# Performance work log

Hardware: AMD Instinct MI355X
Metric: run time of the kernel (lower is better)

Reference implementation:

```python
import jax, jax.numpy as jnp
import numpy as np

BS, SL, H, DH = 2, 2048, 32, 128
STRIDE = 16
NUM_PAGES = BS * (SL // STRIDE)  # 256, distinct page per block
PAGE_DIM = 1 * 2 * STRIDE * H * DH  # blocks * partitions * stride * kv_heads * head_dim


def setup_inputs() -> dict:
    key = jax.random.key(0)
    k1, k2, k3 = jax.random.split(key, 3)
    xq = jax.random.normal(k1, (BS, SL, H, DH), dtype=jnp.float32)
    xk = jax.random.normal(k2, (BS, SL, H, DH), dtype=jnp.float32)
    xv = jax.random.normal(k3, (BS, SL, H, DH), dtype=jnp.float32)
    cache_state = jnp.zeros((NUM_PAGES, PAGE_DIM), dtype=jnp.float32)
    seq_block_ids = jnp.arange(BS * (SL // STRIDE), dtype=jnp.int64 if jax.config.jax_enable_x64 else jnp.int32).reshape(BS, SL // STRIDE)
    return {"xq": xq, "xk": xk, "xv": xv, "cache_state": cache_state, "seq_block_ids": seq_block_ids}


def reference(xq, xk, xv, cache_state, seq_block_ids):
    bs, sl, h, dh = xq.shape
    nb = sl // STRIDE  # blocks per sequence
    num_pages = cache_state.shape[0]

    # --- paged cache write (prefill path: start_positions is None) ---
    # page layout: [page, transformer_block(=1), partition(k=0,v=1), stride, head, head_dim]
    cache = cache_state.reshape(num_pages, 1, 2, STRIDE, h, dh)
    pids = seq_block_ids.reshape(-1)  # [bs*nb]
    k_blocks = xk.reshape(bs * nb, STRIDE, h, dh)
    v_blocks = xv.reshape(bs * nb, STRIDE, h, dh)
    cache = cache.at[pids, 0, 0].set(k_blocks)
    cache = cache.at[pids, 0, 1].set(v_blocks)
    new_cache_state = cache.reshape(cache_state.shape)

    # --- GQA repeat_kv: n_rep = head_count // head_count_kv = 1 -> no-op ---

    # --- SDPA, attn_mask=None, is_causal=False ---
    scale = 1.0 / np.sqrt(dh).astype(np.float32)
    scores = jnp.einsum("bqhd,bkhd->bhqk", xq, xk) * scale  # [bs, h, sl, sl]
    attn = jax.nn.softmax(scores, axis=-1)
    out = jnp.einsum("bhqk,bkhd->bqhd", attn, xv)
    attn_output = out.reshape(bs, sl, h * dh)
    return attn_output, new_cache_state
```

## Files before the change

kernel.cpp:

```cpp
#include <hip/hip_runtime.h>
#include <hip/hip_bf16.h>
#include <stdint.h>

#define BS 2
#define SL 2048
#define H 32
#define DH 128
#define ATT_ELEMS (BS*SL*H*DH)
#define KTILES (SL/64)
#define QSCALE (0.08838834764831845f * 1.4426950408889634f)

typedef __attribute__((ext_vector_type(8))) short short8_t;
typedef __attribute__((ext_vector_type(16))) float f32x16_t;
typedef __attribute__((ext_vector_type(4))) unsigned int u32x4_t;
typedef __attribute__((ext_vector_type(2))) unsigned int u32x2_t;

union FragU { u32x4_t u; short8_t s; };

__device__ __forceinline__ unsigned short f2bf(float x){
    union { float f; unsigned int u; } v; v.f = x;
    unsigned int r = v.u + 0x7fffu + ((v.u >> 16) & 1u);
    return (unsigned short)(r >> 16);
}
__device__ __forceinline__ unsigned int pack2(float a, float b){
    return (unsigned int)f2bf(a) | ((unsigned int)f2bf(b) << 16);
}
__device__ __forceinline__ unsigned int cvtpk(float a, float b){
    unsigned int r;
    asm("v_cvt_pk_bf16_f32 %0, %1, %2" : "=v"(r) : "v"(a), "v"(b));
    return r;
}
__device__ __forceinline__ void gload16(const unsigned short* g, unsigned short* l){
    __builtin_amdgcn_global_load_lds(
        (const __attribute__((address_space(1))) void*)(const void*)g,
        (__attribute__((address_space(3))) void*)(void*)l, 16, 0, 0);
}

__global__ __launch_bounds__(256) void prep_kv_kernel(const float* __restrict__ xk,
                                                      const float* __restrict__ xv,
                                                      const int* __restrict__ pids,
                                                      unsigned short* __restrict__ kfr,
                                                      unsigned short* __restrict__ vfr,
                                                      float* __restrict__ out_cache,
                                                      int do_cache){
    __shared__ unsigned short tK[64*136];
    __shared__ unsigned short tV[64*136];
    int tile = blockIdx.x, h = blockIdx.y, b = blockIdx.z;
    int tid = threadIdx.x;
    size_t tbase = ((size_t)((b*H + h)*KTILES + tile)) * 8192;
    int pg[4];
    #pragma unroll
    for (int j = 0; j < 4; ++j) pg[j] = pids[b*128 + tile*4 + j];

    #pragma unroll
    for (int i = 0; i < 8; ++i){
        int c = tid + 256*i;
        int row = c >> 5, f4 = c & 31;
        size_t gidx = ((size_t)((b*SL + tile*64 + row)*H + h))*DH + f4*4;
        float4 kx = *(const float4*)(xk + gidx);
        float4 vx = *(const float4*)(xv + gidx);
        u32x2_t kw; kw[0] = pack2(kx.x, kx.y); kw[1] = pack2(kx.z, kx.w);
        u32x2_t vw; vw[0] = pack2(vx.x, vx.y); vw[1] = pack2(vx.z, vx.w);
        *(u32x2_t*)(&tK[row*136 + f4*4]) = kw;
        *(u32x2_t*)(&tV[row*136 + f4*4]) = vw;
        if (do_cache){
            size_t cb = (size_t)pg[row>>4]*131072 + (size_t)(row&15)*4096 + h*128 + f4*4;
            *(float4*)(out_cache + cb)         = kx;
            *(float4*)(out_cache + cb + 65536) = vx;
        }
    }
    __syncthreads();
    #pragma unroll
    for (int i = 0; i < 4; ++i){
        int c = tid + 256*i;
        int fi = c >> 6, l = c & 63;
        int key = (fi >> 3)*32 + (l & 31);
        int d0  = (fi & 7)*16 + (l >> 5)*8;
        u32x4_t w = *(const u32x4_t*)(&tK[key*136 + d0]);
        *(u32x4_t*)(&kfr[tbase + (size_t)c*8]) = w;
    }
    #pragma unroll
    for (int i = 0; i < 4; ++i){
        int c = tid + 256*i;
        int fi = c >> 6, l = c & 63;
        int d  = (fi >> 2)*32 + (l & 31);
        int k0 = (fi & 3)*16 + (l >> 5)*8;
        u32x4_t u;
        #pragma unroll
        for (int w = 0; w < 4; ++w)
            u[w] = (unsigned)tV[(k0+2*w)*136 + d] | ((unsigned)tV[(k0+2*w+1)*136 + d] << 16);
        *(u32x4_t*)(&vfr[tbase + (size_t)c*8]) = u;
    }
}

__global__ __launch_bounds__(256) void cache_scatter_kernel(const float* __restrict__ xk,
                                                            const float* __restrict__ xv,
                                                            const int* __restrict__ pids,
                                                            float* __restrict__ out_cache){
    int sb = blockIdx.x >> 1, part = blockIdx.x & 1;
    int page = pids[sb];
    const float4* s4 = (const float4*)((part ? xv : xk) + (size_t)sb * 65536);
    float4* d4 = (float4*)(out_cache + (size_t)page * 131072 + (size_t)part * 65536);
    int base = blockIdx.y * 2048 + threadIdx.x;
    #pragma unroll
    for (int i = 0; i < 8; ++i) d4[base + i*256] = s4[base + i*256];
}

__global__ __launch_bounds__(256, 2) void attn_kernel(const float* __restrict__ xq,
                                                      const unsigned short* __restrict__ kfr,
                                                      const unsigned short* __restrict__ vfr,
                                                      float* __restrict__ out){
    __shared__ unsigned short smem[4*8192];

    const int tid  = threadIdx.x;
    const int lane = tid & 63;
    const int wave = tid >> 6;
    const int l31  = lane & 31;
    const int hi   = lane >> 5;

    int lin = blockIdx.x;
    int swz = (lin & 7)*128 + (lin >> 3);
    const int qblk = swz & 15;
    const int h    = (swz >> 4) & 31;
    const int b    = swz >> 9;
    const int qbase = qblk*128 + wave*32;

    short8_t qf[8];
    {
        const float* qptr = xq + ((size_t)((b*SL + qbase + l31)*H + h))*DH + hi*8;
        #pragma unroll
        for (int f = 0; f < 8; ++f){
            float4 a = *(const float4*)(qptr + f*16);
            float4 c = *(const float4*)(qptr + f*16 + 4);
            FragU w;
            w.u[0] = pack2(a.x*QSCALE, a.y*QSCALE);
            w.u[1] = pack2(a.z*QSCALE, a.w*QSCALE);
            w.u[2] = pack2(c.x*QSCALE, c.y*QSCALE);
            w.u[3] = pack2(c.z*QSCALE, c.w*QSCALE);
            qf[f] = w.s;
        }
    }

    f32x16_t acc[4];
    #pragma unroll
    for (int d = 0; d < 4; ++d)
        #pragma unroll
        for (int r = 0; r < 16; ++r) acc[d][r] = 0.f;
    float m = -1e30f, l_run = 0.f;

    const size_t bh = (size_t)(b*H + h) * (KTILES*8192);
    const unsigned short* kg = kfr + bh;
    const unsigned short* vg = vfr + bh;

    #pragma unroll
    for (int i = 0; i < 4; ++i){
        int ch = wave*4 + i;
        gload16(kg + ch*512 + lane*8, smem + ch*512);
        gload16(vg + ch*512 + lane*8, smem + 16384 + ch*512);
    }
    asm volatile("s_waitcnt vmcnt(0)" ::: "memory");
    __builtin_amdgcn_s_barrier();
    asm volatile("" ::: "memory");

    #pragma unroll 1
    for (int t = 0; t < KTILES; ++t){
        const int p = t & 1;
        unsigned short* Kc = smem + p*8192;
        unsigned short* Vc = smem + 16384 + p*8192;

        if (t + 1 < KTILES){
            const unsigned short* kn = kg + (size_t)(t+1)*8192;
            const unsigned short* vn = vg + (size_t)(t+1)*8192;
            unsigned short* Kn = smem + (p^1)*8192;
            unsigned short* Vn = smem + 16384 + (p^1)*8192;
            #pragma unroll
            for (int i = 0; i < 4; ++i){
                int ch = wave*4 + i;
                gload16(kn + ch*512 + lane*8, Kn + ch*512);
                gload16(vn + ch*512 + lane*8, Vn + ch*512);
            }
        }
        __builtin_amdgcn_sched_barrier(0);

        f32x16_t s0a, s0b, s1a, s1b;
        #pragma unroll
        for (int r = 0; r < 16; ++r){ s0a[r] = 0.f; s0b[r] = 0.f; s1a[r] = 0.f; s1b[r] = 0.f; }
        __builtin_amdgcn_s_setprio(1);
        #pragma unroll
        for (int f = 0; f < 4; ++f){
            FragU k0, k1, k2, k3;
            k0.u = *(const u32x4_t*)(&Kc[(f   )*512 + lane*8]);
            k1.u = *(const u32x4_t*)(&Kc[(8+f )*512 + lane*8]);
            k2.u = *(const u32x4_t*)(&Kc[(4+f )*512 + lane*8]);
            k3.u = *(const u32x4_t*)(&Kc[(12+f)*512 + lane*8]);
            s0a = __builtin_amdgcn_mfma_f32_32x32x16_bf16(k0.s, qf[f],   s0a, 0, 0, 0);
            s1a = __builtin_amdgcn_mfma_f32_32x32x16_bf16(k1.s, qf[f],   s1a, 0, 0, 0);
            s0b = __builtin_amdgcn_mfma_f32_32x32x16_bf16(k2.s, qf[4+f], s0b, 0, 0, 0);
            s1b = __builtin_amdgcn_mfma_f32_32x32x16_bf16(k3.s, qf[4+f], s1b, 0, 0, 0);
        }
        __builtin_amdgcn_s_setprio(0);
        f32x16_t s0 = s0a + s0b;
        f32x16_t s1 = s1a + s1b;

        float t16[16];
        #pragma unroll
        for (int r = 0; r < 16; ++r) t16[r] = fmaxf(s0[r], s1[r]);
        #pragma unroll
        for (int w = 8; w >= 1; w >>= 1)
            #pragma unroll
            for (int r = 0; r < 8; ++r)
                if (r < w) t16[r] = fmaxf(t16[r], t16[r+w]);
        float tmax = fmaxf(t16[0], __shfl_xor(t16[0], 32, 64));

        if (!__all(tmax - m <= 8.f)){
            float mn = fmaxf(m, tmax);
            float corr = __builtin_amdgcn_exp2f(m - mn);
            l_run *= corr;
            float cr[16];
            #pragma unroll
            for (int r = 0; r < 16; ++r)
                cr[r] = __shfl(corr, (r&3) + 8*(r>>2) + 4*hi, 64);
            #pragma unroll
            for (int d = 0; d < 4; ++d)
                #pragma unroll
                for (int r = 0; r < 16; ++r) acc[d][r] *= cr[r];
            m = mn;
        }

        float lsum = 0.f;
        FragU pf[4];
        #define PSLICE(KS, SV, RB)                                                          \
        {                                                                                   \
            float e0 = __builtin_amdgcn_exp2f(SV[RB+0] - m);                                \
            float e1 = __builtin_amdgcn_exp2f(SV[RB+1] - m);                                \
            float e2 = __builtin_amdgcn_exp2f(SV[RB+2] - m);                                \
            float e3 = __builtin_amdgcn_exp2f(SV[RB+3] - m);                                \
            float e4 = __builtin_amdgcn_exp2f(SV[RB+4] - m);                                \
            float e5 = __builtin_amdgcn_exp2f(SV[RB+5] - m);                                \
            float e6 = __builtin_amdgcn_exp2f(SV[RB+6] - m);                                \
            float e7 = __builtin_amdgcn_exp2f(SV[RB+7] - m);                                \
            lsum += ((e0+e1)+(e2+e3)) + ((e4+e5)+(e6+e7));                                  \
            unsigned a  = cvtpk(e0,e1), bq = cvtpk(e2,e3);                                  \
            unsigned cq = cvtpk(e4,e5), dq = cvtpk(e6,e7);                                  \
            unsigned y0 = hi ? a : cq,  y1 = hi ? bq : dq;                                  \
            unsigned r0 = __shfl_xor(y0, 32, 64);                                           \
            unsigned r1 = __shfl_xor(y1, 32, 64);                                           \
            pf[KS].u[0] = hi ? r0 : a;  pf[KS].u[1] = hi ? r1 : bq;                         \
            pf[KS].u[2] = hi ? cq : r0; pf[KS].u[3] = hi ? dq : r1;                         \
        }
        PSLICE(0, s0, 0)
        PSLICE(1, s0, 8)
        PSLICE(2, s1, 0)
        PSLICE(3, s1, 8)
        #undef PSLICE
        lsum += __shfl_xor(lsum, 32, 64);
        l_run += lsum;

        __builtin_amdgcn_s_setprio(1);
        #pragma unroll
        for (int dblk = 0; dblk < 4; ++dblk){
            #pragma unroll
            for (int ks = 0; ks < 4; ++ks){
                FragU vb;
                vb.u = *(const u32x4_t*)(&Vc[(dblk*4 + ks)*512 + lane*8]);
                acc[dblk] = __builtin_amdgcn_mfma_f32_32x32x16_bf16(pf[ks].s, vb.s, acc[dblk], 0, 0, 0);
            }
        }
        __builtin_amdgcn_s_setprio(0);

        if (t + 1 < KTILES){
            asm volatile("s_waitcnt vmcnt(0)" ::: "memory");
            __builtin_amdgcn_s_barrier();
            asm volatile("" ::: "memory");
        }
    }

    float linv = 1.f / l_run;
    float lr[16];
    #pragma unroll
    for (int r = 0; r < 16; ++r)
        lr[r] = __shfl(linv, (r&3) + 8*(r>>2) + 4*hi, 64);
    #pragma unroll
    for (int dblk = 0; dblk < 4; ++dblk){
        #pragma unroll
        for (int r = 0; r < 16; ++r){
            int q = qbase + (r&3) + 8*(r>>2) + 4*hi;
            out[(size_t)(b*SL + q)*(H*DH) + h*DH + dblk*32 + l31] = acc[dblk][r] * lr[r];
        }
    }
}

extern "C" void kernel_launch(void* const* d_in, const int* in_sizes, int n_in,
                              void* d_out, int out_size, void* d_ws, size_t ws_size,
                              hipStream_t stream) {
    const float* xq = (const float*)d_in[0];
    const float* xk = (const float*)d_in[1];
    const float* xv = (const float*)d_in[2];
    const int* pids = (const int*)d_in[4];

    float* out_attn  = (float*)d_out;
    float* out_cache = out_attn + (size_t)ATT_ELEMS;

    const size_t frag_elems = (size_t)BS*H*KTILES*8192;
    const size_t need       = 2*frag_elems*sizeof(unsigned short);

    if (ws_size >= need){
        unsigned short* kfr = (unsigned short*)d_ws;
        unsigned short* vfr = kfr + frag_elems;
        prep_kv_kernel<<<dim3(KTILES, H, BS), 256, 0, stream>>>(xk, xv, pids, kfr, vfr, out_cache, 1);
        attn_kernel<<<dim3(BS*H*(SL/128)), 256, 0, stream>>>(xq, kfr, vfr, out_attn);
    } else {
        unsigned short* vfr = (unsigned short*)out_cache;
        unsigned short* kfr = vfr + frag_elems;
        prep_kv_kernel<<<dim3(KTILES, H, BS), 256, 0, stream>>>(xk, xv, pids, kfr, vfr, out_cache, 0);
        attn_kernel<<<dim3(BS*H*(SL/128)), 256, 0, stream>>>(xq, kfr, vfr, out_attn);
        cache_scatter_kernel<<<dim3(512, 8), 256, 0, stream>>>(xk, xv, pids, out_cache);
    }
}
```

Measured before the change: 236.5 us.

## Halve attention key tile to 32 and raise occupancy to four blocks per CU

Attention now processes keys in tiles of 32 instead of 64, halving the shared-memory double buffer and the score and probability register arrays. Launch bounds move from 2 to 4 blocks per CU, aiming to hide latency through occupancy. The prep kernel's fragment layout is rearranged so each 64-key tile holds two contiguous 32-key sub-tiles. In exchange there are twice as many loop iterations, so more barriers, more softmax max-reductions and more rescale checks per key, and registers may spill under the tighter bound.

```diff
diff --git a/kernel.cpp b/kernel.cpp
--- a/kernel.cpp
+++ b/kernel.cpp
@@ -8,6 +8,7 @@
 #define DH 128
 #define ATT_ELEMS (BS*SL*H*DH)
 #define KTILES (SL/64)
+#define KT32 (SL/32)
 #define QSCALE (0.08838834764831845f * 1.4426950408889634f)
 
 typedef __attribute__((ext_vector_type(8))) short short8_t;
@@ -47,7 +48,7 @@
     __shared__ unsigned short tV[64*136];
     int tile = blockIdx.x, h = blockIdx.y, b = blockIdx.z;
     int tid = threadIdx.x;
-    size_t tbase = ((size_t)((b*H + h)*KTILES + tile)) * 8192;
+    size_t tb = ((size_t)((b*H + h)*KTILES + tile)) * 8192;
     int pg[4];
     #pragma unroll
     for (int j = 0; j < 4; ++j) pg[j] = pids[b*128 + tile*4 + j];
@@ -73,23 +74,25 @@
     #pragma unroll
     for (int i = 0; i < 4; ++i){
         int c = tid + 256*i;
-        int fi = c >> 6, l = c & 63;
-        int key = (fi >> 3)*32 + (l & 31);
-        int d0  = (fi & 7)*16 + (l >> 5)*8;
+        int sub = c >> 9, c2 = c & 511;
+        int fi = c2 >> 6, l = c2 & 63;
+        int key = sub*32 + (l & 31);
+        int d0  = fi*16 + (l >> 5)*8;
         u32x4_t w = *(const u32x4_t*)(&tK[key*136 + d0]);
-        *(u32x4_t*)(&kfr[tbase + (size_t)c*8]) = w;
+        *(u32x4_t*)(&kfr[tb + (size_t)sub*4096 + (size_t)c2*8]) = w;
     }
     #pragma unroll
     for (int i = 0; i < 4; ++i){
         int c = tid + 256*i;
-        int fi = c >> 6, l = c & 63;
-        int d  = (fi >> 2)*32 + (l & 31);
-        int k0 = (fi & 3)*16 + (l >> 5)*8;
+        int sub = c >> 9, c2 = c & 511;
+        int fi = c2 >> 6, l = c2 & 63;
+        int d  = (fi >> 1)*32 + (l & 31);
+        int k0 = sub*32 + (fi & 1)*16 + (l >> 5)*8;
         u32x4_t u;
         #pragma unroll
         for (int w = 0; w < 4; ++w)
             u[w] = (unsigned)tV[(k0+2*w)*136 + d] | ((unsigned)tV[(k0+2*w+1)*136 + d] << 16);
-        *(u32x4_t*)(&vfr[tbase + (size_t)c*8]) = u;
+        *(u32x4_t*)(&vfr[tb + (size_t)sub*4096 + (size_t)c2*8]) = u;
     }
 }
 
@@ -106,11 +109,11 @@
     for (int i = 0; i < 8; ++i) d4[base + i*256] = s4[base + i*256];
 }
 
-__global__ __launch_bounds__(256, 2) void attn_kernel(const float* __restrict__ xq,
+__global__ __launch_bounds__(256, 4) void attn_kernel(const float* __restrict__ xq,
                                                       const unsigned short* __restrict__ kfr,
                                                       const unsigned short* __restrict__ vfr,
                                                       float* __restrict__ out){
-    __shared__ unsigned short smem[4*8192];
+    __shared__ unsigned short smem[4*4096];
 
     const int tid  = threadIdx.x;
     const int lane = tid & 63;
@@ -148,69 +151,64 @@
         for (int r = 0; r < 16; ++r) acc[d][r] = 0.f;
     float m = -1e30f, l_run = 0.f;
 
-    const size_t bh = (size_t)(b*H + h) * (KTILES*8192);
+    const size_t bh = (size_t)(b*H + h) * ((size_t)KT32*4096);
     const unsigned short* kg = kfr + bh;
     const unsigned short* vg = vfr + bh;
 
     #pragma unroll
-    for (int i = 0; i < 4; ++i){
-        int ch = wave*4 + i;
+    for (int i = 0; i < 2; ++i){
+        int ch = wave*2 + i;
         gload16(kg + ch*512 + lane*8, smem + ch*512);
-        gload16(vg + ch*512 + lane*8, smem + 16384 + ch*512);
+        gload16(vg + ch*512 + lane*8, smem + 8192 + ch*512);
     }
     asm volatile("s_waitcnt vmcnt(0)" ::: "memory");
     __builtin_amdgcn_s_barrier();
     asm volatile("" ::: "memory");
 
     #pragma unroll 1
-    for (int t = 0; t < KTILES; ++t){
+    for (int t = 0; t < KT32; ++t){
         const int p = t & 1;
-        unsigned short* Kc = smem + p*8192;
-        unsigned short* Vc = smem + 16384 + p*8192;
-
-        if (t + 1 < KTILES){
-            const unsigned short* kn = kg + (size_t)(t+1)*8192;
-            const unsigned short* vn = vg + (size_t)(t+1)*8192;
-            unsigned short* Kn = smem + (p^1)*8192;
-            unsigned short* Vn = smem + 16384 + (p^1)*8192;
-            #pragma unroll
-            for (int i = 0; i < 4; ++i){
-                int ch = wave*4 + i;
+        unsigned short* Kc = smem + p*4096;
+        unsigned short* Vc = smem + 8192 + p*4096;
+
+        if (t + 1 < KT32){
+            const unsigned short* kn = kg + (size_t)(t+1)*4096;
+            const unsigned short* vn = vg + (size_t)(t+1)*4096;
+            unsigned short* Kn = smem + (p^1)*4096;
+            unsigned short* Vn = smem + 8192 + (p^1)*4096;
+            #pragma unroll
+            for (int i = 0; i < 2; ++i){
+                int ch = wave*2 + i;
                 gload16(kn + ch*512 + lane*8, Kn + ch*512);
                 gload16(vn + ch*512 + lane*8, Vn + ch*512);
             }
         }
         __builtin_amdgcn_sched_barrier(0);
 
-        f32x16_t s0a, s0b, s1a, s1b;
-        #pragma unroll
-        for (int r = 0; r < 16; ++r){ s0a[r] = 0.f; s0b[r] = 0.f; s1a[r] = 0.f; s1b[r] = 0.f; }
+        f32x16_t sa, sb;
+        #pragma unroll
+        for (int r = 0; r < 16; ++r){ sa[r] = 0.f; sb[r] = 0.f; }
         __builtin_amdgcn_s_setprio(1);
         #pragma unroll
         for (int f = 0; f < 4; ++f){
-            FragU k0, k1, k2, k3;
-            k0.u = *(const u32x4_t*)(&Kc[(f   )*512 + lane*8]);
-            k1.u = *(const u32x4_t*)(&Kc[(8+f )*512 + lane*8]);
-            k2.u = *(const u32x4_t*)(&Kc[(4+f )*512 + lane*8]);
-            k3.u = *(const u32x4_t*)(&Kc[(12+f)*512 + lane*8]);
-            s0a = __builtin_amdgcn_mfma_f32_32x32x16_bf16(k0.s, qf[f],   s0a, 0, 0, 0);
-            s1a = __builtin_amdgcn_mfma_f32_32x32x16_bf16(k1.s, qf[f],   s1a, 0, 0, 0);
-            s0b = __builtin_amdgcn_mfma_f32_32x32x16_bf16(k2.s, qf[4+f], s0b, 0, 0, 0);
-            s1b = __builtin_amdgcn_mfma_f32_32x32x16_bf16(k3.s, qf[4+f], s1b, 0, 0, 0);
+            FragU k0, k1;
+            k0.u = *(const u32x4_t*)(&Kc[(f  )*512 + lane*8]);
+            k1.u = *(const u32x4_t*)(&Kc[(4+f)*512 + lane*8]);
+            sa = __builtin_amdgcn_mfma_f32_32x32x16_bf16(k0.s, qf[f],   sa, 0, 0, 0);
+            sb = __builtin_amdgcn_mfma_f32_32x32x16_bf16(k1.s, qf[4+f], sb, 0, 0, 0);
         }
         __builtin_amdgcn_s_setprio(0);
-        f32x16_t s0 = s0a + s0b;
-        f32x16_t s1 = s1a + s1b;
-
-        float t16[16];
-        #pragma unroll
-        for (int r = 0; r < 16; ++r) t16[r] = fmaxf(s0[r], s1[r]);
-        #pragma unroll
-        for (int w = 8; w >= 1; w >>= 1)
-            #pragma unroll
-            for (int r = 0; r < 8; ++r)
-                if (r < w) t16[r] = fmaxf(t16[r], t16[r+w]);
-        float tmax = fmaxf(t16[0], __shfl_xor(t16[0], 32, 64));
+        f32x16_t s = sa + sb;
+
+        float t8[8];
+        #pragma unroll
+        for (int r = 0; r < 8; ++r) t8[r] = fmaxf(s[r], s[8+r]);
+        #pragma unroll
+        for (int w = 4; w >= 1; w >>= 1)
+            #pragma unroll
+            for (int r = 0; r < 4; ++r)
+                if (r < w) t8[r] = fmaxf(t8[r], t8[r+w]);
+        float tmax = fmaxf(t8[0], __shfl_xor(t8[0], 32, 64));
 
         if (!__all(tmax - m <= 8.f)){
             float mn = fmaxf(m, tmax);
@@ -228,17 +226,17 @@
         }
 
         float lsum = 0.f;
-        FragU pf[4];
-        #define PSLICE(KS, SV, RB)                                                          \
+        FragU pf[2];
+        #define PSLICE(KS, RB)                                                              \
         {                                                                                   \
-            float e0 = __builtin_amdgcn_exp2f(SV[RB+0] - m);                                \
-            float e1 = __builtin_amdgcn_exp2f(SV[RB+1] - m);                                \
-            float e2 = __builtin_amdgcn_exp2f(SV[RB+2] - m);                                \
-            float e3 = __builtin_amdgcn_exp2f(SV[RB+3] - m);                                \
-            float e4 = __builtin_amdgcn_exp2f(SV[RB+4] - m);                                \
-            float e5 = __builtin_amdgcn_exp2f(SV[RB+5] - m);                                \
-            float e6 = __builtin_amdgcn_exp2f(SV[RB+6] - m);                                \
-            float e7 = __builtin_amdgcn_exp2f(SV[RB+7] - m);                                \
+            float e0 = __builtin_amdgcn_exp2f(s[RB+0] - m);                                 \
+            float e1 = __builtin_amdgcn_exp2f(s[RB+1] - m);                                 \
+            float e2 = __builtin_amdgcn_exp2f(s[RB+2] - m);                                 \
+            float e3 = __builtin_amdgcn_exp2f(s[RB+3] - m);                                 \
+            float e4 = __builtin_amdgcn_exp2f(s[RB+4] - m);                                 \
+            float e5 = __builtin_amdgcn_exp2f(s[RB+5] - m);                                 \
+            float e6 = __builtin_amdgcn_exp2f(s[RB+6] - m);                                 \
+            float e7 = __builtin_amdgcn_exp2f(s[RB+7] - m);                                 \
             lsum += ((e0+e1)+(e2+e3)) + ((e4+e5)+(e6+e7));                                  \
             unsigned a  = cvtpk(e0,e1), bq = cvtpk(e2,e3);                                  \
             unsigned cq = cvtpk(e4,e5), dq = cvtpk(e6,e7);                                  \
@@ -248,10 +246,8 @@
             pf[KS].u[0] = hi ? r0 : a;  pf[KS].u[1] = hi ? r1 : bq;                         \
             pf[KS].u[2] = hi ? cq : r0; pf[KS].u[3] = hi ? dq : r1;                         \
         }
-        PSLICE(0, s0, 0)
-        PSLICE(1, s0, 8)
-        PSLICE(2, s1, 0)
-        PSLICE(3, s1, 8)
+        PSLICE(0, 0)
+        PSLICE(1, 8)
         #undef PSLICE
         lsum += __shfl_xor(lsum, 32, 64);
         l_run += lsum;
@@ -260,15 +256,15 @@
         #pragma unroll
         for (int dblk = 0; dblk < 4; ++dblk){
             #pragma unroll
-            for (int ks = 0; ks < 4; ++ks){
+            for (int ks = 0; ks < 2; ++ks){
                 FragU vb;
-                vb.u = *(const u32x4_t*)(&Vc[(dblk*4 + ks)*512 + lane*8]);
+                vb.u = *(const u32x4_t*)(&Vc[(dblk*2 + ks)*512 + lane*8]);
                 acc[dblk] = __builtin_amdgcn_mfma_f32_32x32x16_bf16(pf[ks].s, vb.s, acc[dblk], 0, 0, 0);
             }
         }
         __builtin_amdgcn_s_setprio(0);
 
-        if (t + 1 < KTILES){
+        if (t + 1 < KT32){
             asm volatile("s_waitcnt vmcnt(0)" ::: "memory");
             __builtin_amdgcn_s_barrier();
             asm volatile("" ::: "memory");
```

Measured after the change: 311.0 us. +31.5%, slower.
